# Kernel tuning notes

Hardware: AMD Instinct MI355X
Metric: run time of the kernel (lower is better)

Reference implementation:

```python
import jax, jax.numpy as jnp
import numpy as np
from jax import lax


def _conv(x, w, b, pad):
    # x [B,C,H,W], w [O,I,kh,kw] -> [B,O,H,W]
    out = lax.conv_general_dilated(x, w, (1, 1), [(pad, pad), (pad, pad)],
                                   dimension_numbers=('NCHW', 'OIHW', 'NCHW'))
    return out + b[None, :, None, None]


def _warp_all(h, flows):
    # h [B,C,H,W]; flows [B,L,2,H,W]. Matches torch grid_sample(align_corners=True,
    # padding_mode='border') on vgrid = base_grid + (-flow): sample at (xx - fx, yy - fy),
    # coordinates clamped to image borders, bilinear interpolation.
    B, C, H, W = h.shape
    L = flows.shape[1]
    xx = jnp.arange(W, dtype=h.dtype)[None, None, None, :]  # [1,1,1,W]
    yy = jnp.arange(H, dtype=h.dtype)[None, None, :, None]  # [1,1,H,1]
    px = jnp.clip(xx - flows[:, :, 0], 0.0, W - 1)  # [B,L,H,W]
    py = jnp.clip(yy - flows[:, :, 1], 0.0, H - 1)
    x0 = jnp.floor(px)
    y0 = jnp.floor(py)
    x0i = x0.astype(jnp.int32)
    y0i = y0.astype(jnp.int32)
    x1i = jnp.minimum(x0i + 1, W - 1)
    y1i = jnp.minimum(y0i + 1, H - 1)
    wx = px - x0
    wy = py - y0

    def per_batch(img, x0i, x1i, y0i, y1i, wx, wy):
        # img [C,H,W]; index maps [L,H,W]; advanced indexing -> [C,L,H,W]
        g = lambda yi, xi: img[:, yi, xi]
        v = (g(y0i, x0i) * ((1 - wx) * (1 - wy))[None]
             + g(y0i, x1i) * (wx * (1 - wy))[None]
             + g(y1i, x0i) * ((1 - wx) * wy)[None]
             + g(y1i, x1i) * (wx * wy)[None])
        # concat over flows in order: [C,L,H,W] -> [L*C,H,W]
        return v.transpose(1, 0, 2, 3).reshape(L * C, H, W)

    return jax.vmap(per_batch)(h, x0i, x1i, y0i, y1i, wx, wy)  # [B,L*C,H,W]


def setup_inputs() -> dict:
    key = jax.random.key(0)
    ks = jax.random.split(key, 12)
    B, Cin, Ch, H, W, L, K = 8, 8, 64, 128, 128, 5, 3
    s = 0.05
    return {
        'x': jax.random.normal(ks[0], (B, Cin, H, W), jnp.float32),
        'h_prev': jax.random.normal(ks[1], (B, Ch, H, W), jnp.float32),
        'w_i2f': jax.random.normal(ks[2], (32, Cin, 5, 5), jnp.float32) * s,
        'b_i2f': jnp.zeros((32,), jnp.float32),
        'w_h2f': jax.random.normal(ks[3], (32, Ch, 5, 5), jnp.float32) * s,
        'b_h2f': jnp.zeros((32,), jnp.float32),
        'w_flows': jax.random.normal(ks[4], (L * 2, 32, 5, 5), jnp.float32) * s,
        'b_flows': jnp.zeros((L * 2,), jnp.float32),
        'w_i2h': jax.random.normal(ks[5], (Ch * 3, Cin, K, K), jnp.float32) * s,
        'b_i2h': jnp.zeros((Ch * 3,), jnp.float32),
        'w_ret': jax.random.normal(ks[6], (Ch * 3, Ch * L, 1, 1), jnp.float32) * s,
        'b_ret': jnp.zeros((Ch * 3,), jnp.float32),
    }


def reference(x, h_prev, w_i2f, b_i2f, w_h2f, b_h2f, w_flows, b_flows,
              w_i2h, b_i2h, w_ret, b_ret):
    Ch = h_prev.shape[1]
    # flow generator
    f = jnp.tanh(_conv(x, w_i2f, b_i2f, 2) + _conv(h_prev, w_h2f, b_h2f, 2))
    flows = _conv(f, w_flows, b_flows, 2)  # [B, 2L, H, W]
    B, twoL, H, W = flows.shape
    flows = flows.reshape(B, twoL // 2, 2, H, W)  # [B,L,2,H,W]
    warped = _warp_all(h_prev, flows)  # [B, L*Ch, H, W]
    # GRU-style gating
    i2h = _conv(x, w_i2h, b_i2h, w_i2h.shape[-1] // 2)
    h2h = _conv(warped, w_ret, b_ret, 0)
    reset = jax.nn.sigmoid(i2h[:, :Ch] + h2h[:, :Ch])
    update = jax.nn.sigmoid(i2h[:, Ch:2 * Ch] + h2h[:, Ch:2 * Ch])
    new_mem = jnp.tanh(i2h[:, 2 * Ch:] + reset * h2h[:, 2 * Ch:])
    return update * h_prev + (1.0 - update) * new_mem
```

## Files before the change

kernel.cpp:

```cpp
#include <hip/hip_runtime.h>
#include <hip/hip_bf16.h>


#define HW 16384
#define W_ 128

typedef __attribute__((ext_vector_type(8))) short short8;
typedef __attribute__((ext_vector_type(4))) float f32x4;
typedef __attribute__((ext_vector_type(4))) unsigned int u32x4;

__device__ __forceinline__ float sigmoidf_(float z) { return 1.f / (1.f + expf(-z)); }

__device__ __forceinline__ short bf16bits(float v) {
  __hip_bfloat16 bv = __float2bfloat16(v);
  return (short)*reinterpret_cast<unsigned short*>(&bv);
}
__device__ __forceinline__ unsigned int bf16u(float v) {
  __hip_bfloat16 bv = __float2bfloat16(v);
  return (unsigned int)*reinterpret_cast<unsigned short*>(&bv);
}
__device__ __forceinline__ float bfb2f(short s) {
  union { unsigned int u; float f; } cv;
  cv.u = ((unsigned int)(unsigned short)s) << 16;
  return cv.f;
}

__global__ __launch_bounds__(256) void k_transpose(
    const float* __restrict__ h, const float* __restrict__ x,
    __hip_bfloat16* __restrict__ cat, __hip_bfloat16* __restrict__ xT) {
  const int b = blockIdx.y;
  const int wv = threadIdx.x >> 6, l = threadIdx.x & 63;
  const int p = blockIdx.x * 64 + l;
  const int c0 = wv * 24;
  short8 v[3];
#pragma unroll
  for (int q = 0; q < 3; ++q)
#pragma unroll
    for (int k = 0; k < 8; ++k) {
      int c = c0 + q * 8 + k;
      float val = 0.f;
      if (c < 64)      val = h[((size_t)(b * 64 + c) << 14) + p];
      else if (c < 72) val = x[((size_t)(b * 8 + (c - 64)) << 14) + p];
      v[q][k] = bf16bits(val);
    }
  short8* dst = reinterpret_cast<short8*>(cat + ((size_t)b * HW + p) * 96 + c0);
#pragma unroll
  for (int q = 0; q < 3; ++q) dst[q] = v[q];

  short8 xv;
#pragma unroll
  for (int k = 0; k < 8; ++k)
    xv[k] = (wv == 0) ? bf16bits(x[((size_t)(b * 8 + k) << 14) + p]) : (short)0;
  reinterpret_cast<short8*>(xT + ((size_t)b * HW + p) * 32)[wv] = xv;
}

__global__ void k_prep_all(const float* __restrict__ w_i2f,
                           const float* __restrict__ w_h2f,
                           const float* __restrict__ w_flows,
                           const float* __restrict__ w_ret,
                           const float* __restrict__ w_i2h,
                           __hip_bfloat16* __restrict__ pfg,
                           __hip_bfloat16* __restrict__ pfl,
                           __hip_bfloat16* __restrict__ packed,
                           __hip_bfloat16* __restrict__ pih) {
  int t = blockIdx.x * 256 + threadIdx.x;
  if (t < 76800) {
    int i = t & 7, l = (t >> 3) & 63, ot = (t >> 9) & 1, r = t >> 10;
    int ks = r % 3, tap = r / 3;
    int oc = ot * 16 + (l & 15), k = ks * 32 + ((l >> 4) << 3) + i;
    float v = 0.f;
    if (k < 64)      v = w_h2f[(size_t)(oc * 64 + k) * 25 + tap];
    else if (k < 72) v = w_i2f[(size_t)(oc * 8 + (k - 64)) * 25 + tap];
    pfg[t] = __float2bfloat16(v);
    return;
  }
  t -= 76800;
  if (t < 12800) {
    int i = t & 7, l = (t >> 3) & 63, tap = t >> 9;
    int oc = l & 15, k = ((l >> 4) << 3) + i;
    pfl[t] = __float2bfloat16(oc < 10 ? w_flows[(size_t)(oc * 32 + k) * 25 + tap] : 0.f);
    return;
  }
  t -= 12800;
  if (t < 61440) {
    int i = t & 7, l = (t >> 3) & 63, ks = (t >> 9) % 10, mt = t / 5120;
    int m = mt * 16 + (l & 15), k = ks * 32 + ((l >> 4) << 3) + i;
    packed[t] = __float2bfloat16(w_ret[(size_t)m * 320 + k]);
    return;
  }
  t -= 61440;
  if (t < 55296) {
    int i = t & 7, l = (t >> 3) & 63, mt = (t >> 9) % 12, tap = t / 6144;
    int m = mt * 16 + (l & 15), k = ((l >> 4) << 3) + i;
    pih[t] = __float2bfloat16(k < 8 ? w_i2h[(size_t)(m * 8 + k) * 9 + tap] : 0.f);
  }
}

__global__ __launch_bounds__(256) void k_flowgen_mfma(
    const __hip_bfloat16* __restrict__ cat, const __hip_bfloat16* __restrict__ pfg,
    const float* __restrict__ b_i2f, const float* __restrict__ b_h2f,
    __hip_bfloat16* __restrict__ f_T) {
  const int id = blockIdx.x;
  const int b = id & 7, r0 = id >> 3;
  const int y = r0 >> 1, x0 = (r0 & 1) << 6;
  const int wv = threadIdx.x >> 6, l = threadIdx.x & 63;
  const int lr = l & 15, lq = l >> 4;
  const int xa = x0 + wv * 16 + lr;
  const short8* pf = reinterpret_cast<const short8*>(pfg);
  const short8 z8 = {0, 0, 0, 0, 0, 0, 0, 0};

  __shared__ unsigned int s[5 * 68 * 20];

  f32x4 acc[2] = {{0.f, 0.f, 0.f, 0.f}, {0.f, 0.f, 0.f, 0.f}};

  for (int ks = 0; ks < 3; ++ks) {
    __syncthreads();
    for (int c = threadIdx.x; c < 1360; c += 256) {
      int px = c >> 2, part = c & 3;
      int r = px / 68, cc = px - r * 68;
      int gy = min(max(y + r - 2, 0), 127);
      int gx = min(max(x0 + cc - 2, 0), 127);
      u32x4 v = *reinterpret_cast<const u32x4*>(
          cat + ((size_t)b * HW + gy * W_ + gx) * 96 + ks * 32 + part * 8);
      *reinterpret_cast<u32x4*>(s + (r * 68 + cc) * 20 + part * 4) = v;
    }
    __syncthreads();
#pragma unroll
    for (int tap = 0; tap < 25; ++tap) {
      const int dy = tap / 5 - 2, dx = tap % 5 - 2;
      const int yy = y + dy, xx = xa + dx;
      const bool ok = ((unsigned)yy < 128u) && ((unsigned)xx < 128u);
      const int cidx = wv * 16 + lr + dx + 2;
      union { u32x4 u; short8 s8; } cv;
      cv.u = *reinterpret_cast<const u32x4*>(s + ((dy + 2) * 68 + cidx) * 20 + lq * 4);
      short8 af = ok ? cv.s8 : z8;
#pragma unroll
      for (int ot = 0; ot < 2; ++ot) {
        short8 bf = pf[(size_t)(((tap * 3 + ks) << 1) + ot) * 64 + l];
        acc[ot] = __builtin_amdgcn_mfma_f32_16x16x32_bf16(af, bf, acc[ot], 0, 0, 0);
      }
    }
  }

  const int pbase = y * W_ + x0 + wv * 16 + lq * 4;
#pragma unroll
  for (int ot = 0; ot < 2; ++ot) {
    const int oc = ot * 16 + lr;
    const float bias = b_i2f[oc] + b_h2f[oc];
#pragma unroll
    for (int r = 0; r < 4; ++r)
      f_T[((size_t)b * HW + pbase + r) * 32 + oc] =
          __float2bfloat16(tanhf(acc[ot][r] + bias));
  }
}

__global__ __launch_bounds__(256) void k_flows_mfma(
    const __hip_bfloat16* __restrict__ f_T, const __hip_bfloat16* __restrict__ pfl,
    const float* __restrict__ b_flows, float* __restrict__ flows) {
  const int id = blockIdx.x;
  const int b = id & 7, r0 = id >> 3;
  const int y = r0 >> 1, x0 = (r0 & 1) << 6;
  const int wv = threadIdx.x >> 6, l = threadIdx.x & 63;
  const int lr = l & 15, lq = l >> 4;
  const int xa = x0 + wv * 16 + lr;
  const short8* ft8 = reinterpret_cast<const short8*>(f_T + (size_t)b * HW * 32);
  const short8* pf = reinterpret_cast<const short8*>(pfl);
  const short8 z8 = {0, 0, 0, 0, 0, 0, 0, 0};

  f32x4 acc = {0.f, 0.f, 0.f, 0.f};

#pragma unroll
  for (int tap = 0; tap < 25; ++tap) {
    const int dy = tap / 5 - 2, dx = tap % 5 - 2;
    const int yy = y + dy, xx = xa + dx;
    const bool ok = ((unsigned)yy < 128u) && ((unsigned)xx < 128u);
    const int yc = min(max(yy, 0), 127), xc = min(max(xx, 0), 127);
    short8 araw = ft8[(size_t)(yc * W_ + xc) * 4 + lq];
    short8 af = ok ? araw : z8;
    short8 bf = pf[tap * 64 + l];
    acc = __builtin_amdgcn_mfma_f32_16x16x32_bf16(af, bf, acc, 0, 0, 0);
  }

  if (lr < 10) {
    const float bb = b_flows[lr];
    const int p = y * W_ + x0 + wv * 16 + lq * 4;
    f32x4 v = {acc[0] + bb, acc[1] + bb, acc[2] + bb, acc[3] + bb};
    *reinterpret_cast<f32x4*>(flows + ((size_t)(b * 10 + lr) << 14) + p) = v;
  }
}

__global__ __launch_bounds__(256, 4) void k_warp_gemm_gate(
    const __hip_bfloat16* __restrict__ cat, const float* __restrict__ flows,
    const __hip_bfloat16* __restrict__ packed,
    const __hip_bfloat16* __restrict__ pih,
    const __hip_bfloat16* __restrict__ xT,
    const float* __restrict__ h,
    const float* __restrict__ b_i2h, const float* __restrict__ b_ret,
    float* __restrict__ out) {
  const int id = blockIdx.x;
  const int b = id & 7;
  const int p0 = (id >> 3) << 6;
  const int t = threadIdx.x;
  const int wv = t >> 6, l = t & 63;

  __shared__ unsigned int lds[64 * 160];

  {
    const int sub = l >> 3, c8 = l & 7;
    const __hip_bfloat16* cbase = cat + (size_t)b * HW * 96 + c8 * 8;
#pragma unroll
    for (int pass = 0; pass < 2; ++pass) {
      const int pxl = pass * 32 + wv * 8 + sub;
      const int p = p0 + pxl;
      const int ox = p & 127, oy = p >> 7;
      const unsigned int sw = (unsigned)(pxl & 7);

      float fx[5], fy[5];
#pragma unroll
      for (int fl = 0; fl < 5; ++fl) {
        fx[fl] = flows[((size_t)(b * 10 + 2 * fl) << 14) + p];
        fy[fl] = flows[((size_t)(b * 10 + 2 * fl + 1) << 14) + p];
      }
      float w00[5], w01[5], w10[5], w11[5];
      const short8 *q00[5], *q01[5], *q10[5], *q11[5];
#pragma unroll
      for (int fl = 0; fl < 5; ++fl) {
        float px = fminf(fmaxf((float)ox - fx[fl], 0.f), 127.f);
        float py = fminf(fmaxf((float)oy - fy[fl], 0.f), 127.f);
        float x0f = floorf(px), y0f = floorf(py);
        float wx = px - x0f, wy = py - y0f;
        int x0 = (int)x0f, y0 = (int)y0f;
        int x1 = min(x0 + 1, 127), y1 = min(y0 + 1, 127);
        w00[fl] = (1.f - wx) * (1.f - wy); w01[fl] = wx * (1.f - wy);
        w10[fl] = (1.f - wx) * wy;         w11[fl] = wx * wy;
        q00[fl] = reinterpret_cast<const short8*>(cbase + (size_t)(y0 * W_ + x0) * 96);
        q01[fl] = reinterpret_cast<const short8*>(cbase + (size_t)(y0 * W_ + x1) * 96);
        q10[fl] = reinterpret_cast<const short8*>(cbase + (size_t)(y1 * W_ + x0) * 96);
        q11[fl] = reinterpret_cast<const short8*>(cbase + (size_t)(y1 * W_ + x1) * 96);
      }
      short8 v00[5], v01[5], v10[5], v11[5];
#pragma unroll
      for (int fl = 0; fl < 5; ++fl) {
        v00[fl] = *q00[fl]; v01[fl] = *q01[fl];
        v10[fl] = *q10[fl]; v11[fl] = *q11[fl];
      }
#pragma unroll
      for (int fl = 0; fl < 5; ++fl) {
        u32x4 wvv;
#pragma unroll
        for (int kk = 0; kk < 4; ++kk) {
          float a0 = bfb2f(v00[fl][2 * kk]) * w00[fl] + bfb2f(v01[fl][2 * kk]) * w01[fl]
                   + bfb2f(v10[fl][2 * kk]) * w10[fl] + bfb2f(v11[fl][2 * kk]) * w11[fl];
          float a1 = bfb2f(v00[fl][2 * kk + 1]) * w00[fl] + bfb2f(v01[fl][2 * kk + 1]) * w01[fl]
                   + bfb2f(v10[fl][2 * kk + 1]) * w10[fl] + bfb2f(v11[fl][2 * kk + 1]) * w11[fl];
          wvv[kk] = bf16u(a0) | (bf16u(a1) << 16);
        }
        const int g0 = fl * 8 + c8;
        *reinterpret_cast<u32x4*>(lds + pxl * 160 + ((unsigned)(g0 ^ sw) << 2)) = wvv;
      }
    }
  }

  const int y = p0 >> 7, x0 = p0 & 127;
  const int lr = l & 15, lq = l >> 4;

  f32x4 acc[3][4], accm[4];
#pragma unroll
  for (int g = 0; g < 3; ++g)
#pragma unroll
    for (int q = 0; q < 4; ++q) acc[g][q] = {0.f, 0.f, 0.f, 0.f};
#pragma unroll
  for (int q = 0; q < 4; ++q) accm[q] = {0.f, 0.f, 0.f, 0.f};

  {
    const short8* xb = reinterpret_cast<const short8*>(xT + (size_t)b * HW * 32);
    const short8* pi = reinterpret_cast<const short8*>(pih);
    const short8 z8 = {0, 0, 0, 0, 0, 0, 0, 0};
#pragma unroll
    for (int tap = 0; tap < 9; ++tap) {
      const int dy = tap / 3 - 1, dx = tap % 3 - 1;
      const int yy = y + dy;
      const bool yok = (unsigned)yy < 128u;
      const int ycl = min(max(yy, 0), 127);
      short8 bf[3];
#pragma unroll
      for (int g = 0; g < 3; ++g) bf[g] = pi[(size_t)(tap * 12 + g * 4 + wv) * 64 + l];
#pragma unroll
      for (int pt = 0; pt < 4; ++pt) {
        const int xx = x0 + pt * 16 + lr + dx;
        const bool ok = yok && ((unsigned)xx < 128u);
        const int xcl = min(max(xx, 0), 127);
        short8 araw = xb[(size_t)(ycl * W_ + xcl) * 4 + lq];
        short8 af = ok ? araw : z8;
        acc[0][pt] = __builtin_amdgcn_mfma_f32_16x16x32_bf16(af, bf[0], acc[0][pt], 0, 0, 0);
        acc[1][pt] = __builtin_amdgcn_mfma_f32_16x16x32_bf16(af, bf[1], acc[1][pt], 0, 0, 0);
        accm[pt]   = __builtin_amdgcn_mfma_f32_16x16x32_bf16(af, bf[2], accm[pt], 0, 0, 0);
      }
    }
  }

  __syncthreads();

  const short8* bp0 = reinterpret_cast<const short8*>(packed) + (size_t)wv * 640 + l;
  for (int ks = 0; ks < 10; ++ks) {
    short8 af[4];
#pragma unroll
    for (int pt = 0; pt < 4; ++pt) {
      const int row = pt * 16 + lr;
      union { u32x4 u; short8 s; } cv;
      cv.u = *reinterpret_cast<const u32x4*>(
          lds + row * 160 + ((unsigned)(((ks << 2) + lq) ^ (row & 7)) << 2));
      af[pt] = cv.s;
    }
    short8 bf[3];
#pragma unroll
    for (int g = 0; g < 3; ++g) bf[g] = bp0[g * 2560 + ks * 64];
#pragma unroll
    for (int g = 0; g < 3; ++g)
#pragma unroll
      for (int pt = 0; pt < 4; ++pt)
        acc[g][pt] = __builtin_amdgcn_mfma_f32_16x16x32_bf16(af[pt], bf[g],
                                                             acc[g][pt], 0, 0, 0);
  }

  const int c = wv * 16 + lr;
  const float bir = b_i2h[c], biu = b_i2h[64 + c], bim = b_i2h[128 + c];
  const float brr = b_ret[c], bru = b_ret[64 + c], brm = b_ret[128 + c];
  const float* hb = h + ((size_t)(b * 64 + c) << 14);
  float* ob = out + ((size_t)(b * 64 + c) << 14);
#pragma unroll
  for (int pt = 0; pt < 4; ++pt) {
#pragma unroll
    for (int r = 0; r < 4; ++r) {
      const int pixel = p0 + pt * 16 + lq * 4 + r;
      float rg = sigmoidf_(acc[0][pt][r] + bir + brr);
      float ug = sigmoidf_(acc[1][pt][r] + biu + bru);
      float mg = tanhf((accm[pt][r] + bim) + rg * (acc[2][pt][r] + brm));
      ob[pixel] = ug * hb[pixel] + (1.f - ug) * mg;
    }
  }
}

extern "C" void kernel_launch(void* const* d_in, const int* in_sizes, int n_in,
                              void* d_out, int out_size, void* d_ws, size_t ws_size,
                              hipStream_t stream) {
  const float* x       = (const float*)d_in[0];
  const float* h       = (const float*)d_in[1];
  const float* w_i2f   = (const float*)d_in[2];
  const float* b_i2f   = (const float*)d_in[3];
  const float* w_h2f   = (const float*)d_in[4];
  const float* b_h2f   = (const float*)d_in[5];
  const float* w_flows = (const float*)d_in[6];
  const float* b_flows = (const float*)d_in[7];
  const float* w_i2h   = (const float*)d_in[8];
  const float* b_i2h   = (const float*)d_in[9];
  const float* w_ret   = (const float*)d_in[10];
  const float* b_ret   = (const float*)d_in[11];
  float* out           = (float*)d_out;
  char* ws = (char*)d_ws;

  __hip_bfloat16* catT   = (__hip_bfloat16*)(ws);
  __hip_bfloat16* f_T    = (__hip_bfloat16*)(ws + 25165824);
  float* flows           = (float*)(ws + 33554432);
  __hip_bfloat16* xT     = (__hip_bfloat16*)(ws + 38797312);
  __hip_bfloat16* packed = (__hip_bfloat16*)(ws + 63963136);
  __hip_bfloat16* pfg    = (__hip_bfloat16*)(ws + 64086016);
  __hip_bfloat16* pfl    = (__hip_bfloat16*)(ws + 64239616);
  __hip_bfloat16* pih    = (__hip_bfloat16*)(ws + 64265216);

  k_transpose<<<dim3(256, 8), 256, 0, stream>>>(h, x, catT, xT);
  k_prep_all<<<806, 256, 0, stream>>>(w_i2f, w_h2f, w_flows, w_ret, w_i2h,
                                      pfg, pfl, packed, pih);

  k_flowgen_mfma<<<2048, 256, 0, stream>>>(catT, pfg, b_i2f, b_h2f, f_T);
  k_flows_mfma<<<2048, 256, 0, stream>>>(f_T, pfl, b_flows, flows);

  k_warp_gemm_gate<<<2048, 256, 0, stream>>>(catT, flows, packed, pih, xT,
                                             h, b_i2h, b_ret, out);
}
```

Before: 165.1 us.

## Interleave warp gathers with i2h conv MFMA taps to hide gather latency

Restructures the warp/gather phase so each pass issues bilinear gathers for two flows at a time, then runs one i2h conv tap of MFMAs while those loads are in flight, then blends and writes to LDS. The aim is to hide global gather latency behind matrix work and shrink the short8 register arrays from five to two per corner. Launch bounds drop from 4 to 3 waves per SIMD, so the compiler gets more registers in exchange for lower occupancy, which can reduce latency hiding elsewhere.

```diff
diff --git a/kernel.cpp b/kernel.cpp
--- a/kernel.cpp
+++ b/kernel.cpp
@@ -189,7 +189,7 @@
   }
 }
 
-__global__ __launch_bounds__(256, 4) void k_warp_gemm_gate(
+__global__ __launch_bounds__(256, 3) void k_warp_gemm_gate(
     const __hip_bfloat16* __restrict__ cat, const float* __restrict__ flows,
     const __hip_bfloat16* __restrict__ packed,
     const __hip_bfloat16* __restrict__ pih,
@@ -202,102 +202,113 @@
   const int p0 = (id >> 3) << 6;
   const int t = threadIdx.x;
   const int wv = t >> 6, l = t & 63;
+  const int lr = l & 15, lq = l >> 4;
+  const int y = p0 >> 7, x0c = p0 & 127;
 
   __shared__ unsigned int lds[64 * 160];
 
-  {
-    const int sub = l >> 3, c8 = l & 7;
-    const __hip_bfloat16* cbase = cat + (size_t)b * HW * 96 + c8 * 8;
-#pragma unroll
-    for (int pass = 0; pass < 2; ++pass) {
-      const int pxl = pass * 32 + wv * 8 + sub;
-      const int p = p0 + pxl;
-      const int ox = p & 127, oy = p >> 7;
-      const unsigned int sw = (unsigned)(pxl & 7);
-
-      float fx[5], fy[5];
-#pragma unroll
-      for (int fl = 0; fl < 5; ++fl) {
-        fx[fl] = flows[((size_t)(b * 10 + 2 * fl) << 14) + p];
-        fy[fl] = flows[((size_t)(b * 10 + 2 * fl + 1) << 14) + p];
+  f32x4 acc[3][4], accm[4];
+#pragma unroll
+  for (int g = 0; g < 3; ++g)
+#pragma unroll
+    for (int q = 0; q < 4; ++q) acc[g][q] = {0.f, 0.f, 0.f, 0.f};
+#pragma unroll
+  for (int q = 0; q < 4; ++q) accm[q] = {0.f, 0.f, 0.f, 0.f};
+
+  const short8* xb = reinterpret_cast<const short8*>(xT + (size_t)b * HW * 32);
+  const short8* pi = reinterpret_cast<const short8*>(pih);
+  const short8 z8 = {0, 0, 0, 0, 0, 0, 0, 0};
+
+  auto do_tap = [&](int tap) {
+    const int dy = tap / 3 - 1, dx = tap % 3 - 1;
+    const int yy = y + dy;
+    const bool yok = (unsigned)yy < 128u;
+    const int ycl = min(max(yy, 0), 127);
+    short8 bf[3];
+#pragma unroll
+    for (int g = 0; g < 3; ++g) bf[g] = pi[(size_t)(tap * 12 + g * 4 + wv) * 64 + l];
+#pragma unroll
+    for (int pt = 0; pt < 4; ++pt) {
+      const int xx = x0c + pt * 16 + lr + dx;
+      const bool ok = yok && ((unsigned)xx < 128u);
+      const int xcl = min(max(xx, 0), 127);
+      short8 araw = xb[(size_t)(ycl * W_ + xcl) * 4 + lq];
+      short8 af = ok ? araw : z8;
+      acc[0][pt] = __builtin_amdgcn_mfma_f32_16x16x32_bf16(af, bf[0], acc[0][pt], 0, 0, 0);
+      acc[1][pt] = __builtin_amdgcn_mfma_f32_16x16x32_bf16(af, bf[1], acc[1][pt], 0, 0, 0);
+      accm[pt]   = __builtin_amdgcn_mfma_f32_16x16x32_bf16(af, bf[2], accm[pt], 0, 0, 0);
+    }
+  };
+
+  const int sub = l >> 3, c8 = l & 7;
+  const __hip_bfloat16* cbase = cat + (size_t)b * HW * 96 + c8 * 8;
+  float w00[5], w01[5], w10[5], w11[5];
+  int o00[5], o01[5], o10[5], o11[5];
+  int pxl = 0, p = 0;
+  unsigned int sw = 0;
+  short8 v00[2], v01[2], v10[2], v11[2];
+
+  auto setup_pass = [&](int pass) {
+    pxl = pass * 32 + wv * 8 + sub;
+    p = p0 + pxl;
+    const int ox = p & 127, oy = p >> 7;
+    sw = (unsigned)(pxl & 7);
+#pragma unroll
+    for (int fl = 0; fl < 5; ++fl) {
+      float fx = flows[((size_t)(b * 10 + 2 * fl) << 14) + p];
+      float fy = flows[((size_t)(b * 10 + 2 * fl + 1) << 14) + p];
+      float px = fminf(fmaxf((float)ox - fx, 0.f), 127.f);
+      float py = fminf(fmaxf((float)oy - fy, 0.f), 127.f);
+      float x0f = floorf(px), y0f = floorf(py);
+      float wx = px - x0f, wy = py - y0f;
+      int x0 = (int)x0f, y0 = (int)y0f;
+      int x1 = min(x0 + 1, 127), y1 = min(y0 + 1, 127);
+      w00[fl] = (1.f - wx) * (1.f - wy); w01[fl] = wx * (1.f - wy);
+      w10[fl] = (1.f - wx) * wy;         w11[fl] = wx * wy;
+      o00[fl] = (y0 * W_ + x0) * 96; o01[fl] = (y0 * W_ + x1) * 96;
+      o10[fl] = (y1 * W_ + x0) * 96; o11[fl] = (y1 * W_ + x1) * 96;
+    }
+  };
+
+  auto issue = [&](int f0, int nf) {
+#pragma unroll
+    for (int j = 0; j < 2; ++j)
+      if (j < nf) {
+        v00[j] = *reinterpret_cast<const short8*>(cbase + o00[f0 + j]);
+        v01[j] = *reinterpret_cast<const short8*>(cbase + o01[f0 + j]);
+        v10[j] = *reinterpret_cast<const short8*>(cbase + o10[f0 + j]);
+        v11[j] = *reinterpret_cast<const short8*>(cbase + o11[f0 + j]);
       }
-      float w00[5], w01[5], w10[5], w11[5];
-      const short8 *q00[5], *q01[5], *q10[5], *q11[5];
-#pragma unroll
-      for (int fl = 0; fl < 5; ++fl) {
-        float px = fminf(fmaxf((float)ox - fx[fl], 0.f), 127.f);
-        float py = fminf(fmaxf((float)oy - fy[fl], 0.f), 127.f);
-        float x0f = floorf(px), y0f = floorf(py);
-        float wx = px - x0f, wy = py - y0f;
-        int x0 = (int)x0f, y0 = (int)y0f;
-        int x1 = min(x0 + 1, 127), y1 = min(y0 + 1, 127);
-        w00[fl] = (1.f - wx) * (1.f - wy); w01[fl] = wx * (1.f - wy);
-        w10[fl] = (1.f - wx) * wy;         w11[fl] = wx * wy;
-        q00[fl] = reinterpret_cast<const short8*>(cbase + (size_t)(y0 * W_ + x0) * 96);
-        q01[fl] = reinterpret_cast<const short8*>(cbase + (size_t)(y0 * W_ + x1) * 96);
-        q10[fl] = reinterpret_cast<const short8*>(cbase + (size_t)(y1 * W_ + x0) * 96);
-        q11[fl] = reinterpret_cast<const short8*>(cbase + (size_t)(y1 * W_ + x1) * 96);
-      }
-      short8 v00[5], v01[5], v10[5], v11[5];
-#pragma unroll
-      for (int fl = 0; fl < 5; ++fl) {
-        v00[fl] = *q00[fl]; v01[fl] = *q01[fl];
-        v10[fl] = *q10[fl]; v11[fl] = *q11[fl];
-      }
-#pragma unroll
-      for (int fl = 0; fl < 5; ++fl) {
+  };
+
+  auto consume = [&](int f0, int nf) {
+#pragma unroll
+    for (int j = 0; j < 2; ++j)
+      if (j < nf) {
+        const int fl = f0 + j;
         u32x4 wvv;
 #pragma unroll
         for (int kk = 0; kk < 4; ++kk) {
-          float a0 = bfb2f(v00[fl][2 * kk]) * w00[fl] + bfb2f(v01[fl][2 * kk]) * w01[fl]
-                   + bfb2f(v10[fl][2 * kk]) * w10[fl] + bfb2f(v11[fl][2 * kk]) * w11[fl];
-          float a1 = bfb2f(v00[fl][2 * kk + 1]) * w00[fl] + bfb2f(v01[fl][2 * kk + 1]) * w01[fl]
-                   + bfb2f(v10[fl][2 * kk + 1]) * w10[fl] + bfb2f(v11[fl][2 * kk + 1]) * w11[fl];
+          float a0 = bfb2f(v00[j][2 * kk]) * w00[fl] + bfb2f(v01[j][2 * kk]) * w01[fl]
+                   + bfb2f(v10[j][2 * kk]) * w10[fl] + bfb2f(v11[j][2 * kk]) * w11[fl];
+          float a1 = bfb2f(v00[j][2 * kk + 1]) * w00[fl] + bfb2f(v01[j][2 * kk + 1]) * w01[fl]
+                   + bfb2f(v10[j][2 * kk + 1]) * w10[fl] + bfb2f(v11[j][2 * kk + 1]) * w11[fl];
           wvv[kk] = bf16u(a0) | (bf16u(a1) << 16);
         }
         const int g0 = fl * 8 + c8;
         *reinterpret_cast<u32x4*>(lds + pxl * 160 + ((unsigned)(g0 ^ sw) << 2)) = wvv;
       }
-    }
-  }
-
-  const int y = p0 >> 7, x0 = p0 & 127;
-  const int lr = l & 15, lq = l >> 4;
-
-  f32x4 acc[3][4], accm[4];
-#pragma unroll
-  for (int g = 0; g < 3; ++g)
-#pragma unroll
-    for (int q = 0; q < 4; ++q) acc[g][q] = {0.f, 0.f, 0.f, 0.f};
-#pragma unroll
-  for (int q = 0; q < 4; ++q) accm[q] = {0.f, 0.f, 0.f, 0.f};
-
-  {
-    const short8* xb = reinterpret_cast<const short8*>(xT + (size_t)b * HW * 32);
-    const short8* pi = reinterpret_cast<const short8*>(pih);
-    const short8 z8 = {0, 0, 0, 0, 0, 0, 0, 0};
-#pragma unroll
-    for (int tap = 0; tap < 9; ++tap) {
-      const int dy = tap / 3 - 1, dx = tap % 3 - 1;
-      const int yy = y + dy;
-      const bool yok = (unsigned)yy < 128u;
-      const int ycl = min(max(yy, 0), 127);
-      short8 bf[3];
-#pragma unroll
-      for (int g = 0; g < 3; ++g) bf[g] = pi[(size_t)(tap * 12 + g * 4 + wv) * 64 + l];
-#pragma unroll
-      for (int pt = 0; pt < 4; ++pt) {
-        const int xx = x0 + pt * 16 + lr + dx;
-        const bool ok = yok && ((unsigned)xx < 128u);
-        const int xcl = min(max(xx, 0), 127);
-        short8 araw = xb[(size_t)(ycl * W_ + xcl) * 4 + lq];
-        short8 af = ok ? araw : z8;
-        acc[0][pt] = __builtin_amdgcn_mfma_f32_16x16x32_bf16(af, bf[0], acc[0][pt], 0, 0, 0);
-        acc[1][pt] = __builtin_amdgcn_mfma_f32_16x16x32_bf16(af, bf[1], acc[1][pt], 0, 0, 0);
-        accm[pt]   = __builtin_amdgcn_mfma_f32_16x16x32_bf16(af, bf[2], accm[pt], 0, 0, 0);
-      }
-    }
-  }
+  };
+
+  setup_pass(0);
+  issue(0, 2); do_tap(0); consume(0, 2);
+  issue(2, 2); do_tap(1); consume(2, 2);
+  issue(4, 1); do_tap(2); consume(4, 1);
+  setup_pass(1);
+  issue(0, 2); do_tap(3); consume(0, 2);
+  issue(2, 2); do_tap(4); consume(2, 2);
+  issue(4, 1); do_tap(5); consume(4, 1);
+  do_tap(6); do_tap(7); do_tap(8);
 
   __syncthreads();
 
```

Result: slower. 178.5 us (+8.1%).
